# Optimization experiments

Measured on AMD Instinct MI355X. Metric: run time of the kernel, lower is better.

The kernel has to match this reference:

```python
import jax, jax.numpy as jnp
import numpy as np

B, S, D, H = 2, 2048, 768, 12
DK = D // H
NEG = -1e9

def setup_inputs() -> dict:
    key = jax.random.key(0)
    ks = jax.random.split(key, 12)
    def lin(k):
        kw, kb = jax.random.split(k)
        lim = 1.0 / np.sqrt(D)
        W = jax.random.uniform(kw, (D, D), jnp.float32, -lim, lim)
        b = jax.random.uniform(kb, (D,), jnp.float32, -lim, lim)
        return W, b
    Wq, bq = lin(ks[0]); Wk, bk = lin(ks[1]); Wv, bv = lin(ks[2]); Wo, bo = lin(ks[3])
    query = jax.random.normal(ks[4], (B, S, D), jnp.float32)
    key_t = jax.random.normal(ks[5], (B, S, D), jnp.float32)
    value = jax.random.normal(ks[6], (B, S, D), jnp.float32)
    mask = jax.random.randint(ks[7], (B, S, S), 0, 2, jnp.int32)
    return {"query": query, "key": key_t, "value": value, "mask": mask,
            "Wq": Wq, "bq": bq, "Wk": Wk, "bk": bk, "Wv": Wv, "bv": bv,
            "Wo": Wo, "bo": bo}

def reference(query, key, value, mask, Wq, bq, Wk, bk, Wv, bv, Wo, bo):
    # project and split heads: [B,S,D] -> [B,H,S,DK]
    def proj(x, W, b):
        return (x @ W.T + b).reshape(B, S, H, DK).transpose(0, 2, 1, 3)
    q = proj(query, Wq, bq)
    k = proj(key, Wk, bk)
    v = proj(value, Wv, bv)
    scale = np.float32(1.0 / np.sqrt(DK))
    scores = jnp.einsum('bhqd,bhkd->bhqk', q, k) * scale  # [B,H,S,S]
    scores = jnp.where(mask[:, None, :, :] == 0, jnp.float32(NEG), scores)
    log_attn = jax.nn.log_softmax(scores, axis=-1)  # [B,H,S,S]
    p_attn = jnp.exp(log_attn)                      # softmax, shares reduction
    x = jnp.einsum('bhqk,bhkd->bhqd', p_attn, v)    # [B,H,S,DK]
    x = x.transpose(0, 2, 1, 3).reshape(B, S, D)
    out = x @ Wo.T + bo
    return out, log_attn
```

## Files before the change

### kernel.cpp

```cpp
#include <hip/hip_runtime.h>

#define B_ 2
#define S_ 2048
#define D_ 768
#define H_ 12
#define DK_ 64
#define BH_ (B_*H_)
#define NEGV (-1e9f)
#define SCALE 0.125f
#define MINIT (-1e30f)

typedef unsigned short u16;
typedef unsigned long long u64;
typedef __attribute__((ext_vector_type(8))) short bf16x8;
typedef __attribute__((ext_vector_type(4))) float f32x4;

__device__ __forceinline__ u16 f2bf(float f){
  union { float f; unsigned int i; } v; v.f = f;
  unsigned int x = v.i;
  return (u16)((x + 0x7FFFu + ((x >> 16) & 1u)) >> 16);
}
__device__ __forceinline__ void split2(float x, u16& h, u16& l){
  const unsigned int xi = __float_as_uint(x);
  h = (u16)(xi >> 16);
  const float lo = x - __uint_as_float(xi & 0xFFFF0000u);
  l = (u16)(__float_as_uint(lo) >> 16);
}

#define XN_ ((size_t)4096*768)
#define WN_ ((size_t)768*768)

__global__ __launch_bounds__(256) void prep(
    const float* __restrict__ Xq, const float* __restrict__ Xk, const float* __restrict__ Xv,
    const float* __restrict__ Wq, const float* __restrict__ Wk, const float* __restrict__ Wv,
    u16* __restrict__ scr)
{
  const int a = blockIdx.y;
  const float* src; u16* h; u16* l; size_t n;
  if (a < 3){
    src = (a==0)?Xq:(a==1)?Xk:Xv;
    h = scr + (size_t)a*XN_;  l = scr + (size_t)(3+a)*XN_;  n = XN_;
  } else {
    const int z = a-3;
    src = (z==0)?Wq:(z==1)?Wk:Wv;
    h = scr + 6*XN_ + (size_t)z*WN_;  l = scr + 6*XN_ + 3*WN_ + (size_t)z*WN_;  n = WN_;
  }
  const size_t nv = n >> 2;
  for (size_t i = (size_t)blockIdx.x*256 + threadIdx.x; i < nv; i += (size_t)gridDim.x*256){
    float4 v = ((const float4*)src)[i];
    ushort4 hv, lv;
    split2(v.x,hv.x,lv.x); split2(v.y,hv.y,lv.y); split2(v.z,hv.z,lv.z); split2(v.w,hv.w,lv.w);
    ((ushort4*)h)[i] = hv;  ((ushort4*)l)[i] = lv;
  }
}

__global__ __launch_bounds__(256) void maskpack(const int* __restrict__ mask, u64* __restrict__ mbits){
  const size_t nw = (size_t)B_*S_*(S_/64);
  for (size_t wi = (size_t)blockIdx.x*256 + threadIdx.x; wi < nw; wi += (size_t)gridDim.x*256){
    const int* mp = mask + wi*64;
    u64 v = 0;
    #pragma unroll
    for (int j=0;j<64;j+=4){
      int4 m4 = *(const int4*)(mp + j);
      v |= ((u64)(m4.x!=0) << j)     | ((u64)(m4.y!=0) << (j+1))
         | ((u64)(m4.z!=0) << (j+2)) | ((u64)(m4.w!=0) << (j+3));
    }
    mbits[wi] = v;
  }
}

template<bool ALO, bool BPRE, int OMODE>
__device__ __forceinline__ void gemmM(const u16* __restrict__ Ah_, const u16* __restrict__ Al_,
                                      const u16* __restrict__ Bh_, const u16* __restrict__ Bl_,
                                      const float* __restrict__ Bf_,
                                      const float* __restrict__ bias, void* __restrict__ outp)
{
  const int bx = blockIdx.x, by = blockIdx.y;
  const int tid  = threadIdx.x;
  const int lane = tid & 63;
  const int w    = tid >> 6;
  const int g    = lane >> 4;
  const int c    = lane & 15;
  const int wr   = w >> 1, wc = w & 1;

  __shared__ u16 Ah[128][36];
  __shared__ u16 Al[128][36];
  __shared__ u16 Bh[128][36];
  __shared__ u16 Bl[128][36];

  const int ar0 = (OMODE==2 ? by : bx) * 128;
  const int br0 = (OMODE==2 ? bx : by) * 128;

  const int prow = tid >> 2;
  const int pcol = (tid & 3) * 8;
  const int frow = tid >> 3;
  const int fcol = (tid & 7) * 4;

  uint4 rAh0, rAh1, rAl0, rAl1, rBh0, rBh1, rBl0, rBl1;
  float4 rf0, rf1, rf2, rf3;

  f32x4 acc[4][4];
  #pragma unroll
  for (int m=0;m<4;m++)
    #pragma unroll
    for (int n=0;n<4;n++) acc[m][n] = (f32x4){0.f,0.f,0.f,0.f};

#define LD_TILE(k0) do{ \
    rAh0 = *(const uint4*)(Ah_ + (size_t)(ar0+prow)*D_ + (k0) + pcol); \
    rAh1 = *(const uint4*)(Ah_ + (size_t)(ar0+64+prow)*D_ + (k0) + pcol); \
    if constexpr (ALO){ \
      rAl0 = *(const uint4*)(Al_ + (size_t)(ar0+prow)*D_ + (k0) + pcol); \
      rAl1 = *(const uint4*)(Al_ + (size_t)(ar0+64+prow)*D_ + (k0) + pcol); } \
    if constexpr (BPRE){ \
      rBh0 = *(const uint4*)(Bh_ + (size_t)(br0+prow)*D_ + (k0) + pcol); \
      rBh1 = *(const uint4*)(Bh_ + (size_t)(br0+64+prow)*D_ + (k0) + pcol); \
      rBl0 = *(const uint4*)(Bl_ + (size_t)(br0+prow)*D_ + (k0) + pcol); \
      rBl1 = *(const uint4*)(Bl_ + (size_t)(br0+64+prow)*D_ + (k0) + pcol); \
    } else { \
      rf0 = *(const float4*)(Bf_ + (size_t)(br0+frow)*D_ + (k0) + fcol); \
      rf1 = *(const float4*)(Bf_ + (size_t)(br0+32+frow)*D_ + (k0) + fcol); \
      rf2 = *(const float4*)(Bf_ + (size_t)(br0+64+frow)*D_ + (k0) + fcol); \
      rf3 = *(const float4*)(Bf_ + (size_t)(br0+96+frow)*D_ + (k0) + fcol); \
    } }while(0)

#define ST_F32(rf, rofs) do{ \
    ushort4 hv, lv; \
    split2((rf).x,hv.x,lv.x); split2((rf).y,hv.y,lv.y); \
    split2((rf).z,hv.z,lv.z); split2((rf).w,hv.w,lv.w); \
    *(ushort4*)&Bh[(rofs)+frow][fcol] = hv;  *(ushort4*)&Bl[(rofs)+frow][fcol] = lv; }while(0)

#define ST_TILE() do{ \
    *(uint4*)&Ah[prow][pcol] = rAh0;  *(uint4*)&Ah[prow+64][pcol] = rAh1; \
    if constexpr (ALO){ *(uint4*)&Al[prow][pcol] = rAl0; *(uint4*)&Al[prow+64][pcol] = rAl1; } \
    if constexpr (BPRE){ \
      *(uint4*)&Bh[prow][pcol] = rBh0;  *(uint4*)&Bh[prow+64][pcol] = rBh1; \
      *(uint4*)&Bl[prow][pcol] = rBl0;  *(uint4*)&Bl[prow+64][pcol] = rBl1; \
    } else { ST_F32(rf0,0); ST_F32(rf1,32); ST_F32(rf2,64); ST_F32(rf3,96); } }while(0)

  LD_TILE(0);

  for (int t=0; t<D_/32; ++t){
    __syncthreads();
    ST_TILE();
    if (t < D_/32 - 1) LD_TILE((t+1)*32);
    __syncthreads();

    bf16x8 fah[4], fal[4], fbh[4], fbl[4];
    #pragma unroll
    for (int m=0;m<4;m++){
      fah[m] = *(const bf16x8*)&Ah[wr*64 + m*16 + c][g*8];
      if constexpr (ALO) fal[m] = *(const bf16x8*)&Al[wr*64 + m*16 + c][g*8];
    }
    #pragma unroll
    for (int n=0;n<4;n++){
      fbh[n] = *(const bf16x8*)&Bh[wc*64 + n*16 + c][g*8];
      fbl[n] = *(const bf16x8*)&Bl[wc*64 + n*16 + c][g*8];
    }
    #pragma unroll
    for (int m=0;m<4;m++)
      #pragma unroll
      for (int n=0;n<4;n++){
        acc[m][n] = __builtin_amdgcn_mfma_f32_16x16x32_bf16(fah[m], fbh[n], acc[m][n], 0,0,0);
        acc[m][n] = __builtin_amdgcn_mfma_f32_16x16x32_bf16(fah[m], fbl[n], acc[m][n], 0,0,0);
        if constexpr (ALO)
          acc[m][n] = __builtin_amdgcn_mfma_f32_16x16x32_bf16(fal[m], fbh[n], acc[m][n], 0,0,0);
      }
  }
#undef LD_TILE
#undef ST_F32
#undef ST_TILE

  if constexpr (OMODE==0) {
    float* out = (float*)outp;
    float bb[4];
    #pragma unroll
    for (int n=0;n<4;n++) bb[n] = bias[br0 + wc*64 + n*16 + c];
    #pragma unroll
    for (int m=0;m<4;m++)
      #pragma unroll
      for (int r=0;r<4;r++){
        const int rg = ar0 + wr*64 + m*16 + g*4 + r;
        #pragma unroll
        for (int n=0;n<4;n++)
          out[(size_t)rg*D_ + br0 + wc*64 + n*16 + c] = acc[m][n][r] + bb[n];
      }
  } else if constexpr (OMODE==1) {
    u16* out = (u16*)outp;
    float bb[4];
    #pragma unroll
    for (int n=0;n<4;n++) bb[n] = bias[br0 + wc*64 + n*16 + c];
    #pragma unroll
    for (int m=0;m<4;m++)
      #pragma unroll
      for (int r=0;r<4;r++){
        const int rg = ar0 + wr*64 + m*16 + g*4 + r;
        const int batch = rg >> 11, s = rg & (S_-1);
        #pragma unroll
        for (int n=0;n<4;n++){
          const int col = br0 + wc*64 + n*16 + c;
          const int hh = col >> 6, dk = col & 63;
          out[((size_t)(batch*H_ + hh)*S_ + s)*DK_ + dk] = f2bf(acc[m][n][r] + bb[n]);
        }
      }
  } else {
    u16* out = (u16*)outp;
    #pragma unroll
    for (int m=0;m<4;m++)
      #pragma unroll
      for (int r=0;r<4;r++){
        const int dkg = ar0 + wr*64 + m*16 + g*4 + r;
        const int hh = dkg >> 6, dkl = dkg & 63;
        const float bb = bias[dkg];
        #pragma unroll
        for (int n=0;n<4;n++){
          const int sg = br0 + wc*64 + n*16 + c;
          const int batch = sg >> 11, s = sg & (S_-1);
          out[((size_t)(batch*H_ + hh)*DK_ + dkl)*S_ + s] = f2bf(acc[m][n][r] + bb);
        }
      }
  }
}

__global__ __launch_bounds__(256,2) void proj_qkv(
    const u16* __restrict__ scr,
    const float* __restrict__ bq, const float* __restrict__ bk, const float* __restrict__ bv,
    u16* __restrict__ qkv)
{
  const int z = blockIdx.z;
  u16* out = qkv + (size_t)z * ((size_t)BH_*S_*DK_);
  const u16* Xh = scr + (size_t)z*XN_;
  const u16* Xl = scr + (size_t)(3+z)*XN_;
  const u16* Wh = scr + 6*XN_ + (size_t)z*WN_;
  const u16* Wl = scr + 6*XN_ + 3*WN_ + (size_t)z*WN_;
  const float* bias = (z==0)?bq:(z==1)?bk:bv;
  if (z==2) gemmM<true,true,2>(Wh, Wl, Xh, Xl, nullptr, bias, (void*)out);
  else      gemmM<true,true,1>(Xh, Xl, Wh, Wl, nullptr, bias, (void*)out);
}

__global__ __launch_bounds__(256,2) void proj_o(
    const u16* __restrict__ Xc, const float* __restrict__ Wo, const float* __restrict__ bo,
    float* __restrict__ out)
{
  gemmM<false,false,0>(Xc, nullptr, nullptr, nullptr, Wo, bo, (void*)out);
}

__global__ __launch_bounds__(256,3) void attn(const u16* __restrict__ qkv,
                                              const u64* __restrict__ mbits,
                                              float* __restrict__ la, u16* __restrict__ ctx)
{
  const int bh = blockIdx.y;
  const int q0 = blockIdx.x * 64;
  const int b = bh / H_;
  const int h = bh - b*H_;
  const u16* Qp = qkv + (size_t)bh * S_ * DK_;
  const u16* Kp = qkv + (size_t)(BH_ + bh) * S_ * DK_;
  const u16* Vt = qkv + (size_t)(2*BH_ + bh) * S_ * DK_;
  const u64* Mb = mbits + (size_t)b * S_ * (S_/64);

  const int tid  = threadIdx.x;
  const int w    = tid >> 6;
  const int lane = tid & 63;
  const int g    = lane >> 4;
  const int c    = lane & 15;
  const int srow = tid >> 3;
  const int scol = (tid & 7) * 8;

  __shared__ u16 KsB[2][64][72];
  __shared__ u16 VsB[2][64][72];
  __shared__ u16 Ps[4][16][72];

  {
    uint4 qa = *(const uint4*)(Qp + (size_t)(q0+srow)*DK_ + scol);
    uint4 qb = *(const uint4*)(Qp + (size_t)(q0+32+srow)*DK_ + scol);
    *(uint4*)&VsB[0][srow][scol] = qa;
    *(uint4*)&VsB[0][srow+32][scol] = qb;
  }
  __syncthreads();
  const bf16x8 qf0 = *(const bf16x8*)&VsB[0][w*16 + c][g*8];
  const bf16x8 qf1 = *(const bf16x8*)&VsB[0][w*16 + c][g*8 + 32];

  float mt[4], lt[4];
  #pragma unroll
  for (int r=0;r<4;r++){ mt[r] = MINIT; lt[r] = 0.f; }

  {
    uint4 ka = *(const uint4*)(Kp + (size_t)srow*DK_ + scol);
    uint4 kb = *(const uint4*)(Kp + (size_t)(32+srow)*DK_ + scol);
    *(uint4*)&KsB[0][srow][scol] = ka;
    *(uint4*)&KsB[0][srow+32][scol] = kb;
    for (int t=0; t<S_/64; ++t){
      __syncthreads();
      if (t < S_/64-1){
        const u16* kp = Kp + (size_t)(t+1)*64*DK_;
        ka = *(const uint4*)(kp + (size_t)srow*DK_ + scol);
        kb = *(const uint4*)(kp + (size_t)(32+srow)*DK_ + scol);
      }
      u64 mw[4];
      #pragma unroll
      for (int r=0;r<4;r++) mw[r] = Mb[(size_t)(q0 + w*16 + g*4 + r)*(S_/64) + t];

      f32x4 sc[4];
      #pragma unroll
      for (int nt=0; nt<4; nt++){
        const bf16x8 kf0 = *(const bf16x8*)&KsB[t&1][nt*16 + c][g*8];
        const bf16x8 kf1 = *(const bf16x8*)&KsB[t&1][nt*16 + c][g*8 + 32];
        f32x4 z = {0.f,0.f,0.f,0.f};
        z      = __builtin_amdgcn_mfma_f32_16x16x32_bf16(qf0, kf0, z, 0,0,0);
        sc[nt] = __builtin_amdgcn_mfma_f32_16x16x32_bf16(qf1, kf1, z, 0,0,0);
      }
      #pragma unroll
      for (int r=0;r<4;r++){
        const float sv0 = ((mw[r] >> (c    )) & 1) ? sc[0][r]*SCALE : NEGV;
        const float sv1 = ((mw[r] >> (c+16)) & 1) ? sc[1][r]*SCALE : NEGV;
        const float sv2 = ((mw[r] >> (c+32)) & 1) ? sc[2][r]*SCALE : NEGV;
        const float sv3 = ((mw[r] >> (c+48)) & 1) ? sc[3][r]*SCALE : NEGV;
        const float cm = fmaxf(fmaxf(sv0,sv1), fmaxf(sv2,sv3));
        if (!__all(cm <= mt[r])){
          const float mn = fmaxf(mt[r], cm);
          lt[r] *= __expf(mt[r]-mn);
          mt[r] = mn;
        }
        lt[r] += __expf(sv0-mt[r]) + __expf(sv1-mt[r]) + __expf(sv2-mt[r]) + __expf(sv3-mt[r]);
      }
      if (t < S_/64-1){
        *(uint4*)&KsB[(t+1)&1][srow][scol] = ka;
        *(uint4*)&KsB[(t+1)&1][srow+32][scol] = kb;
      }
    }
  }

  float ml[4];
  #pragma unroll
  for (int r=0;r<4;r++){
    float m = mt[r], l = lt[r];
    #pragma unroll
    for (int st=1; st<16; st<<=1){
      const float m2 = __shfl_xor(m, st);
      const float l2 = __shfl_xor(l, st);
      const float mn = fmaxf(m, m2);
      l = l*__expf(m-mn) + l2*__expf(m2-mn);
      m = mn;
    }
    ml[r] = m + __logf(fmaxf(l, 1e-30f));
  }

  f32x4 o[4];
  #pragma unroll
  for (int nt=0;nt<4;nt++) o[nt] = (f32x4){0.f,0.f,0.f,0.f};

  {
    uint4 ka = *(const uint4*)(Kp + (size_t)srow*DK_ + scol);
    uint4 kb = *(const uint4*)(Kp + (size_t)(32+srow)*DK_ + scol);
    uint4 va = *(const uint4*)(Vt + (size_t)srow*S_ + scol);
    uint4 vb = *(const uint4*)(Vt + (size_t)(32+srow)*S_ + scol);
    *(uint4*)&KsB[0][srow][scol] = ka;   *(uint4*)&KsB[0][srow+32][scol] = kb;
    *(uint4*)&VsB[0][srow][scol] = va;   *(uint4*)&VsB[0][srow+32][scol] = vb;
    for (int t=0; t<S_/64; ++t){
      __syncthreads();
      if (t < S_/64-1){
        const u16* kp = Kp + (size_t)(t+1)*64*DK_;
        const u16* vp = Vt + (size_t)(t+1)*64;
        ka = *(const uint4*)(kp + (size_t)srow*DK_ + scol);
        kb = *(const uint4*)(kp + (size_t)(32+srow)*DK_ + scol);
        va = *(const uint4*)(vp + (size_t)srow*S_ + scol);
        vb = *(const uint4*)(vp + (size_t)(32+srow)*S_ + scol);
      }
      u64 mw[4];
      #pragma unroll
      for (int r=0;r<4;r++) mw[r] = Mb[(size_t)(q0 + w*16 + g*4 + r)*(S_/64) + t];

      f32x4 sc[4];
      #pragma unroll
      for (int nt=0; nt<4; nt++){
        const bf16x8 kf0 = *(const bf16x8*)&KsB[t&1][nt*16 + c][g*8];
        const bf16x8 kf1 = *(const bf16x8*)&KsB[t&1][nt*16 + c][g*8 + 32];
        f32x4 z = {0.f,0.f,0.f,0.f};
        z      = __builtin_amdgcn_mfma_f32_16x16x32_bf16(qf0, kf0, z, 0,0,0);
        sc[nt] = __builtin_amdgcn_mfma_f32_16x16x32_bf16(qf1, kf1, z, 0,0,0);
      }
      float lvv[4][4];
      #pragma unroll
      for (int r=0;r<4;r++){
        #pragma unroll
        for (int nt=0;nt<4;nt++){
          const float s  = ((mw[r] >> (nt*16 + c)) & 1) ? sc[nt][r]*SCALE : NEGV;
          const float lv = fminf(s - ml[r], 0.f);
          lvv[r][nt] = lv;
          Ps[w][g*4+r][nt*16 + c] = f2bf(__expf(lv));
        }
      }
      const bf16x8 pf0 = *(const bf16x8*)&Ps[w][c][g*8];
      const bf16x8 pf1 = *(const bf16x8*)&Ps[w][c][g*8 + 32];
      #pragma unroll
      for (int nt=0; nt<4; nt++){
        const bf16x8 vf0 = *(const bf16x8*)&VsB[t&1][nt*16 + c][g*8];
        const bf16x8 vf1 = *(const bf16x8*)&VsB[t&1][nt*16 + c][g*8 + 32];
        o[nt] = __builtin_amdgcn_mfma_f32_16x16x32_bf16(pf0, vf0, o[nt], 0,0,0);
        o[nt] = __builtin_amdgcn_mfma_f32_16x16x32_bf16(pf1, vf1, o[nt], 0,0,0);
      }
      #pragma unroll
      for (int r=0;r<4;r++){
        float* lrow = la + ((size_t)bh*S_ + q0 + w*16 + g*4 + r)*S_ + (size_t)t*64 + c;
        #pragma unroll
        for (int nt=0;nt<4;nt++) lrow[nt*16] = lvv[r][nt];
      }
      if (t < S_/64-1){
        *(uint4*)&KsB[(t+1)&1][srow][scol] = ka;   *(uint4*)&KsB[(t+1)&1][srow+32][scol] = kb;
        *(uint4*)&VsB[(t+1)&1][srow][scol] = va;   *(uint4*)&VsB[(t+1)&1][srow+32][scol] = vb;
      }
    }
  }

  #pragma unroll
  for (int r=0;r<4;r++){
    const int qi = q0 + w*16 + g*4 + r;
    u16* crow = ctx + ((size_t)b*S_ + qi)*D_ + h*DK_ + c;
    #pragma unroll
    for (int nt=0;nt<4;nt++) crow[nt*16] = f2bf(o[nt][r]);
  }
}

extern "C" void kernel_launch(void* const* d_in, const int* in_sizes, int n_in,
                              void* d_out, int out_size, void* d_ws, size_t ws_size,
                              hipStream_t stream)
{
  const float* query = (const float*)d_in[0];
  const float* key   = (const float*)d_in[1];
  const float* value = (const float*)d_in[2];
  const int* mask    = (const int*)d_in[3];
  const float* Wq = (const float*)d_in[4];  const float* bq = (const float*)d_in[5];
  const float* Wk = (const float*)d_in[6];  const float* bk = (const float*)d_in[7];
  const float* Wv = (const float*)d_in[8];  const float* bv = (const float*)d_in[9];
  const float* Wo = (const float*)d_in[10]; const float* bo = (const float*)d_in[11];

  float* out = (float*)d_out;
  float* la  = out + (size_t)B_*S_*D_;
  u16* qkvws = (u16*)d_ws;
  u16* ctx = qkvws + (size_t)3*BH_*S_*DK_;
  u16* scr = (u16*)la;
  u64* mbits = (u64*)out;

  prep    <<<dim3(768,6,1),    dim3(256,1,1), 0, stream>>>(query,key,value,Wq,Wk,Wv,scr);
  maskpack<<<dim3(512,1,1),    dim3(256,1,1), 0, stream>>>(mask, mbits);
  proj_qkv<<<dim3(32,6,3),     dim3(256,1,1), 0, stream>>>(scr, bq,bk,bv, qkvws);
  attn    <<<dim3(S_/64,BH_,1),dim3(256,1,1), 0, stream>>>(qkvws, mbits, la, ctx);
  proj_o  <<<dim3(32,6,1),     dim3(256,1,1), 0, stream>>>(ctx, Wo, bo, out);
}
```

Before: 648.2 us.

## Widen attention blocks to 128 queries, fuse maskpack into prep, add MFMA priority hints

Attention blocks now use 512 threads covering 128 query rows, so each K/V tile loaded into shared memory serves twice as many queries. Each thread loads one row chunk instead of two, and the Q staging is moved into KsB. The mask-packing kernel is merged into prep as an extra grid slice, removing one launch. Nontemporal loads/stores are added for streaming inputs and the log_attn output, and s_setprio brackets around the MFMA sections. The larger block raises register and LDS pressure per CU and reduces the number of blocks.

Result: slower. 697.0 us (+7.5%).

```diff
diff --git a/kernel.cpp b/kernel.cpp
--- a/kernel.cpp
+++ b/kernel.cpp
@@ -14,6 +14,7 @@
 typedef unsigned long long u64;
 typedef __attribute__((ext_vector_type(8))) short bf16x8;
 typedef __attribute__((ext_vector_type(4))) float f32x4;
+typedef __attribute__((ext_vector_type(4))) int   i32x4;
 
 __device__ __forceinline__ u16 f2bf(float f){
   union { float f; unsigned int i; } v; v.f = f;
@@ -33,9 +34,25 @@
 __global__ __launch_bounds__(256) void prep(
     const float* __restrict__ Xq, const float* __restrict__ Xk, const float* __restrict__ Xv,
     const float* __restrict__ Wq, const float* __restrict__ Wk, const float* __restrict__ Wv,
-    u16* __restrict__ scr)
+    const int* __restrict__ mask,
+    u16* __restrict__ scr, u64* __restrict__ mbits)
 {
   const int a = blockIdx.y;
+  if (a == 6){
+    const size_t nw = (size_t)B_*S_*(S_/64);
+    for (size_t wi = (size_t)blockIdx.x*256 + threadIdx.x; wi < nw; wi += (size_t)gridDim.x*256){
+      const int* mp = mask + wi*64;
+      u64 v = 0;
+      #pragma unroll
+      for (int j=0;j<64;j+=4){
+        i32x4 m4 = __builtin_nontemporal_load((const i32x4*)(mp + j));
+        v |= ((u64)(m4.x!=0) << j)     | ((u64)(m4.y!=0) << (j+1))
+           | ((u64)(m4.z!=0) << (j+2)) | ((u64)(m4.w!=0) << (j+3));
+      }
+      mbits[wi] = v;
+    }
+    return;
+  }
   const float* src; u16* h; u16* l; size_t n;
   if (a < 3){
     src = (a==0)?Xq:(a==1)?Xk:Xv;
@@ -47,25 +64,10 @@
   }
   const size_t nv = n >> 2;
   for (size_t i = (size_t)blockIdx.x*256 + threadIdx.x; i < nv; i += (size_t)gridDim.x*256){
-    float4 v = ((const float4*)src)[i];
+    f32x4 v = __builtin_nontemporal_load((const f32x4*)src + i);
     ushort4 hv, lv;
     split2(v.x,hv.x,lv.x); split2(v.y,hv.y,lv.y); split2(v.z,hv.z,lv.z); split2(v.w,hv.w,lv.w);
     ((ushort4*)h)[i] = hv;  ((ushort4*)l)[i] = lv;
-  }
-}
-
-__global__ __launch_bounds__(256) void maskpack(const int* __restrict__ mask, u64* __restrict__ mbits){
-  const size_t nw = (size_t)B_*S_*(S_/64);
-  for (size_t wi = (size_t)blockIdx.x*256 + threadIdx.x; wi < nw; wi += (size_t)gridDim.x*256){
-    const int* mp = mask + wi*64;
-    u64 v = 0;
-    #pragma unroll
-    for (int j=0;j<64;j+=4){
-      int4 m4 = *(const int4*)(mp + j);
-      v |= ((u64)(m4.x!=0) << j)     | ((u64)(m4.y!=0) << (j+1))
-         | ((u64)(m4.z!=0) << (j+2)) | ((u64)(m4.w!=0) << (j+3));
-    }
-    mbits[wi] = v;
   }
 }
 
@@ -156,6 +158,7 @@
       fbh[n] = *(const bf16x8*)&Bh[wc*64 + n*16 + c][g*8];
       fbl[n] = *(const bf16x8*)&Bl[wc*64 + n*16 + c][g*8];
     }
+    __builtin_amdgcn_s_setprio(1);
     #pragma unroll
     for (int m=0;m<4;m++)
       #pragma unroll
@@ -165,6 +168,7 @@
         if constexpr (ALO)
           acc[m][n] = __builtin_amdgcn_mfma_f32_16x16x32_bf16(fal[m], fbh[n], acc[m][n], 0,0,0);
       }
+    __builtin_amdgcn_s_setprio(0);
   }
 #undef LD_TILE
 #undef ST_F32
@@ -244,12 +248,12 @@
   gemmM<false,false,0>(Xc, nullptr, nullptr, nullptr, Wo, bo, (void*)out);
 }
 
-__global__ __launch_bounds__(256,3) void attn(const u16* __restrict__ qkv,
+__global__ __launch_bounds__(512,4) void attn(const u16* __restrict__ qkv,
                                               const u64* __restrict__ mbits,
                                               float* __restrict__ la, u16* __restrict__ ctx)
 {
   const int bh = blockIdx.y;
-  const int q0 = blockIdx.x * 64;
+  const int q0 = blockIdx.x * 128;
   const int b = bh / H_;
   const int h = bh - b*H_;
   const u16* Qp = qkv + (size_t)bh * S_ * DK_;
@@ -267,17 +271,20 @@
 
   __shared__ u16 KsB[2][64][72];
   __shared__ u16 VsB[2][64][72];
-  __shared__ u16 Ps[4][16][72];
+  __shared__ u16 Ps[8][16][72];
 
   {
     uint4 qa = *(const uint4*)(Qp + (size_t)(q0+srow)*DK_ + scol);
-    uint4 qb = *(const uint4*)(Qp + (size_t)(q0+32+srow)*DK_ + scol);
-    *(uint4*)&VsB[0][srow][scol] = qa;
-    *(uint4*)&VsB[0][srow+32][scol] = qb;
+    uint4 qb = *(const uint4*)(Qp + (size_t)(q0+64+srow)*DK_ + scol);
+    *(uint4*)&KsB[0][srow][scol] = qa;
+    *(uint4*)&KsB[1][srow][scol] = qb;
   }
   __syncthreads();
-  const bf16x8 qf0 = *(const bf16x8*)&VsB[0][w*16 + c][g*8];
-  const bf16x8 qf1 = *(const bf16x8*)&VsB[0][w*16 + c][g*8 + 32];
+  const u16 (*QT)[72] = (w < 4) ? KsB[0] : KsB[1];
+  const int qr = (w & 3)*16 + c;
+  const bf16x8 qf0 = *(const bf16x8*)&QT[qr][g*8];
+  const bf16x8 qf1 = *(const bf16x8*)&QT[qr][g*8 + 32];
+  __syncthreads();
 
   float mt[4], lt[4];
   #pragma unroll
@@ -285,21 +292,17 @@
 
   {
     uint4 ka = *(const uint4*)(Kp + (size_t)srow*DK_ + scol);
-    uint4 kb = *(const uint4*)(Kp + (size_t)(32+srow)*DK_ + scol);
     *(uint4*)&KsB[0][srow][scol] = ka;
-    *(uint4*)&KsB[0][srow+32][scol] = kb;
     for (int t=0; t<S_/64; ++t){
       __syncthreads();
-      if (t < S_/64-1){
-        const u16* kp = Kp + (size_t)(t+1)*64*DK_;
-        ka = *(const uint4*)(kp + (size_t)srow*DK_ + scol);
-        kb = *(const uint4*)(kp + (size_t)(32+srow)*DK_ + scol);
-      }
+      if (t < S_/64-1)
+        ka = *(const uint4*)(Kp + (size_t)((t+1)*64+srow)*DK_ + scol);
       u64 mw[4];
       #pragma unroll
       for (int r=0;r<4;r++) mw[r] = Mb[(size_t)(q0 + w*16 + g*4 + r)*(S_/64) + t];
 
       f32x4 sc[4];
+      __builtin_amdgcn_s_setprio(1);
       #pragma unroll
       for (int nt=0; nt<4; nt++){
         const bf16x8 kf0 = *(const bf16x8*)&KsB[t&1][nt*16 + c][g*8];
@@ -308,6 +311,7 @@
         z      = __builtin_amdgcn_mfma_f32_16x16x32_bf16(qf0, kf0, z, 0,0,0);
         sc[nt] = __builtin_amdgcn_mfma_f32_16x16x32_bf16(qf1, kf1, z, 0,0,0);
       }
+      __builtin_amdgcn_s_setprio(0);
       #pragma unroll
       for (int r=0;r<4;r++){
         const float sv0 = ((mw[r] >> (c    )) & 1) ? sc[0][r]*SCALE : NEGV;
@@ -322,10 +326,8 @@
         }
         lt[r] += __expf(sv0-mt[r]) + __expf(sv1-mt[r]) + __expf(sv2-mt[r]) + __expf(sv3-mt[r]);
       }
-      if (t < S_/64-1){
+      if (t < S_/64-1)
         *(uint4*)&KsB[(t+1)&1][srow][scol] = ka;
-        *(uint4*)&KsB[(t+1)&1][srow+32][scol] = kb;
-      }
     }
   }
 
@@ -350,26 +352,21 @@
 
   {
     uint4 ka = *(const uint4*)(Kp + (size_t)srow*DK_ + scol);
-    uint4 kb = *(const uint4*)(Kp + (size_t)(32+srow)*DK_ + scol);
     uint4 va = *(const uint4*)(Vt + (size_t)srow*S_ + scol);
-    uint4 vb = *(const uint4*)(Vt + (size_t)(32+srow)*S_ + scol);
-    *(uint4*)&KsB[0][srow][scol] = ka;   *(uint4*)&KsB[0][srow+32][scol] = kb;
-    *(uint4*)&VsB[0][srow][scol] = va;   *(uint4*)&VsB[0][srow+32][scol] = vb;
+    *(uint4*)&KsB[0][srow][scol] = ka;
+    *(uint4*)&VsB[0][srow][scol] = va;
     for (int t=0; t<S_/64; ++t){
       __syncthreads();
       if (t < S_/64-1){
-        const u16* kp = Kp + (size_t)(t+1)*64*DK_;
-        const u16* vp = Vt + (size_t)(t+1)*64;
-        ka = *(const uint4*)(kp + (size_t)srow*DK_ + scol);
-        kb = *(const uint4*)(kp + (size_t)(32+srow)*DK_ + scol);
-        va = *(const uint4*)(vp + (size_t)srow*S_ + scol);
-        vb = *(const uint4*)(vp + (size_t)(32+srow)*S_ + scol);
+        ka = *(const uint4*)(Kp + (size_t)((t+1)*64+srow)*DK_ + scol);
+        va = *(const uint4*)(Vt + (size_t)srow*S_ + (t+1)*64 + scol);
       }
       u64 mw[4];
       #pragma unroll
       for (int r=0;r<4;r++) mw[r] = Mb[(size_t)(q0 + w*16 + g*4 + r)*(S_/64) + t];
 
       f32x4 sc[4];
+      __builtin_amdgcn_s_setprio(1);
       #pragma unroll
       for (int nt=0; nt<4; nt++){
         const bf16x8 kf0 = *(const bf16x8*)&KsB[t&1][nt*16 + c][g*8];
@@ -378,19 +375,21 @@
         z      = __builtin_amdgcn_mfma_f32_16x16x32_bf16(qf0, kf0, z, 0,0,0);
         sc[nt] = __builtin_amdgcn_mfma_f32_16x16x32_bf16(qf1, kf1, z, 0,0,0);
       }
-      float lvv[4][4];
+      __builtin_amdgcn_s_setprio(0);
       #pragma unroll
       for (int r=0;r<4;r++){
+        float* lrow = la + ((size_t)bh*S_ + q0 + w*16 + g*4 + r)*S_ + (size_t)t*64 + c;
         #pragma unroll
         for (int nt=0;nt<4;nt++){
           const float s  = ((mw[r] >> (nt*16 + c)) & 1) ? sc[nt][r]*SCALE : NEGV;
           const float lv = fminf(s - ml[r], 0.f);
-          lvv[r][nt] = lv;
           Ps[w][g*4+r][nt*16 + c] = f2bf(__expf(lv));
+          __builtin_nontemporal_store(lv, lrow + nt*16);
         }
       }
       const bf16x8 pf0 = *(const bf16x8*)&Ps[w][c][g*8];
       const bf16x8 pf1 = *(const bf16x8*)&Ps[w][c][g*8 + 32];
+      __builtin_amdgcn_s_setprio(1);
       #pragma unroll
       for (int nt=0; nt<4; nt++){
         const bf16x8 vf0 = *(const bf16x8*)&VsB[t&1][nt*16 + c][g*8];
@@ -398,15 +397,10 @@
         o[nt] = __builtin_amdgcn_mfma_f32_16x16x32_bf16(pf0, vf0, o[nt], 0,0,0);
         o[nt] = __builtin_amdgcn_mfma_f32_16x16x32_bf16(pf1, vf1, o[nt], 0,0,0);
       }
-      #pragma unroll
-      for (int r=0;r<4;r++){
-        float* lrow = la + ((size_t)bh*S_ + q0 + w*16 + g*4 + r)*S_ + (size_t)t*64 + c;
-        #pragma unroll
-        for (int nt=0;nt<4;nt++) lrow[nt*16] = lvv[r][nt];
-      }
+      __builtin_amdgcn_s_setprio(0);
       if (t < S_/64-1){
-        *(uint4*)&KsB[(t+1)&1][srow][scol] = ka;   *(uint4*)&KsB[(t+1)&1][srow+32][scol] = kb;
-        *(uint4*)&VsB[(t+1)&1][srow][scol] = va;   *(uint4*)&VsB[(t+1)&1][srow+32][scol] = vb;
+        *(uint4*)&KsB[(t+1)&1][srow][scol] = ka;
+        *(uint4*)&VsB[(t+1)&1][srow][scol] = va;
       }
     }
   }
@@ -440,9 +434,8 @@
   u16* scr = (u16*)la;
   u64* mbits = (u64*)out;
 
-  prep    <<<dim3(768,6,1),    dim3(256,1,1), 0, stream>>>(query,key,value,Wq,Wk,Wv,scr);
-  maskpack<<<dim3(512,1,1),    dim3(256,1,1), 0, stream>>>(mask, mbits);
-  proj_qkv<<<dim3(32,6,3),     dim3(256,1,1), 0, stream>>>(scr, bq,bk,bv, qkvws);
-  attn    <<<dim3(S_/64,BH_,1),dim3(256,1,1), 0, stream>>>(qkvws, mbits, la, ctx);
-  proj_o  <<<dim3(32,6,1),     dim3(256,1,1), 0, stream>>>(ctx, Wo, bo, out);
-}
+  prep    <<<dim3(768,7,1),     dim3(256,1,1), 0, stream>>>(query,key,value,Wq,Wk,Wv,mask,scr,mbits);
+  proj_qkv<<<dim3(32,6,3),      dim3(256,1,1), 0, stream>>>(scr, bq,bk,bv, qkvws);
+  attn    <<<dim3(S_/128,BH_,1),dim3(512,1,1), 0, stream>>>(qkvws, mbits, la, ctx);
+  proj_o  <<<dim3(32,6,1),      dim3(256,1,1), 0, stream>>>(ctx, Wo, bo, out);
+}
```
